# Kernel optimization log

Measured on AMD Instinct MI355X. Metric: run time of the kernel, lower is better.

## Reference

```python
import jax, jax.numpy as jnp
import numpy as np

EMB = 2048
N_HEADS = 16
HEAD_DIM = EMB // N_HEADS
ROPE_BASE = 10000.0


def _rope_cos_sin(seq_len, head_dim, dtype):
    inv_freq = 1.0 / (ROPE_BASE ** (jnp.arange(0, head_dim, 2, dtype=jnp.float32) / head_dim))
    t = jnp.arange(seq_len, dtype=jnp.float32)
    freqs = jnp.einsum('s,d->sd', t, inv_freq)          # [S, head_dim/2]
    emb = jnp.concatenate([freqs, freqs], axis=-1)       # [S, head_dim]
    return jnp.cos(emb).astype(dtype), jnp.sin(emb).astype(dtype)


def _rotate_half(x):
    x1, x2 = jnp.split(x, 2, axis=-1)
    return jnp.concatenate([-x2, x1], axis=-1)


def _apply_rope(x, cos, sin):
    # x: [B, H, S, D]; cos/sin: [S, D]
    return x * cos[None, None, :, :] + _rotate_half(x) * sin[None, None, :, :]


def setup_inputs() -> dict:
    key = jax.random.key(0)
    k1, k2, k3 = jax.random.split(key, 3)
    B, S = 4, 2048
    x = jax.random.normal(k1, (B, S, EMB), dtype=jnp.float32)
    # Additive causal mask: 0 on/below diagonal, -1e9 above.
    causal = jnp.triu(jnp.full((S, S), -1e9, dtype=jnp.float32), k=1)
    att_mask = causal[None, None, :, :]
    Wqkv = jax.random.normal(k2, (3 * EMB, EMB), dtype=jnp.float32) * (EMB ** -0.5)
    Wout = jax.random.normal(k3, (EMB, EMB), dtype=jnp.float32) * (EMB ** -0.5)
    return {"x": x, "att_mask": att_mask, "Wqkv": Wqkv, "Wout": Wout}


def reference(x, att_mask, Wqkv, Wout):
    B, S, E = x.shape
    qkv = jnp.einsum('bse,fe->bsf', x, Wqkv)             # [B, S, 3E]
    q, k, v = jnp.split(qkv, 3, axis=-1)
    def to_heads(t):
        return t.reshape(B, S, N_HEADS, HEAD_DIM).transpose(0, 2, 1, 3)  # [B,H,S,D]
    q, k, v = to_heads(q), to_heads(k), to_heads(v)
    cos, sin = _rope_cos_sin(S, HEAD_DIM, x.dtype)
    q = _apply_rope(q, cos, sin)
    k = _apply_rope(k, cos, sin)
    scaling = HEAD_DIM ** -0.5
    dots = jnp.einsum('bhqd,bhkd->bhqk', q, k) * scaling
    dots = dots + att_mask
    attn = jax.nn.softmax(dots, axis=-1)
    out = jnp.einsum('bhqk,bhkd->bhqd', attn, v)         # [B,H,S,D]
    out = out.transpose(0, 2, 1, 3).reshape(B, S, E)
    return jnp.einsum('bse,fe->bsf', out, Wout)
```

## Files before the change

### kernel.cpp

```cpp
#include <hip/hip_runtime.h>
#include <stdint.h>

typedef __attribute__((ext_vector_type(8))) short short8_t;
typedef __attribute__((ext_vector_type(4))) float f32x4;

__device__ __forceinline__ short f2bf(float f) {
  union { float f; uint32_t u; } v; v.f = f;
  uint32_t r = v.u + 0x7FFFu + ((v.u >> 16) & 1u);
  return (short)(r >> 16);
}
__device__ __forceinline__ float bf2f(short s) {
  union { uint32_t u; float f; } v; v.u = ((uint32_t)(uint16_t)s) << 16; return v.f;
}
__device__ __forceinline__ void gld16(const void* g, void* l) {
  __builtin_amdgcn_global_load_lds((const __attribute__((address_space(1))) void*)g,
                                   (__attribute__((address_space(3))) void*)l, 16, 0, 0);
}

__global__ __launch_bounds__(256) void conv3_kernel(const float* __restrict__ x,
                                                    const float* __restrict__ wqkv,
                                                    const float* __restrict__ wout,
                                                    short* __restrict__ xb,
                                                    short* __restrict__ wqb,
                                                    short* __restrict__ woutb) {
  int i = blockIdx.x * 256 + threadIdx.x;
  const int stride = gridDim.x * 256;
  for (; i < 8388608; i += stride) {
    const float4* src;
    short4* dst;
    int j;
    if (i < 4194304) { src = (const float4*)x; dst = (short4*)xb; j = i; }
    else if (i < 7340032) { src = (const float4*)wqkv; dst = (short4*)wqb; j = i - 4194304; }
    else { src = (const float4*)wout; dst = (short4*)woutb; j = i - 7340032; }
    float4 v = src[j];
    short4 o;
    o.x = f2bf(v.x); o.y = f2bf(v.y); o.z = f2bf(v.z); o.w = f2bf(v.w);
    dst[j] = o;
  }
}

__device__ __forceinline__ void storeC(float* C, size_t i, float v) { C[i] = v; }
__device__ __forceinline__ void storeC(short* C, size_t i, float v) { C[i] = f2bf(v); }

template <typename OT, bool FUSEV>
__global__ __launch_bounds__(512, 2) void gemm8p(const short* __restrict__ A,
                                                 const short* __restrict__ B,
                                                 OT* __restrict__ C,
                                                 short* __restrict__ VT,
                                                 int M, int N, int K) {
  __shared__ __align__(16) short lds[65536];
  const int tid = threadIdx.x, lane = tid & 63, w = tid >> 6;
  const int wr = w >> 2, wc = w & 3;
  const int c = lane & 15, g4 = lane >> 4;
  const int xcd = (int)blockIdx.x & 7;
  const int t = (int)blockIdx.x >> 3;
  const int bx = (t & 7) + 8 * (t >> 5);
  const int by = xcd * 4 + ((t >> 3) & 3);
  const size_t m0 = (size_t)by * 256, n0 = (size_t)bx * 256;
  const size_t Kb = (size_t)K * 2;
  const char* Ab = (const char*)A + m0 * Kb;
  const char* Bb = (const char*)B + n0 * Kb;
  const char* aq[2];
  const char* bq[2];
#pragma unroll
  for (int i = 0; i < 2; ++i) {
    const size_t ro = (size_t)((i * 8 + w) * 16 + c) * Kb + g4 * 16;
    aq[i] = Ab + ro;
    bq[i] = Bb + ro;
  }
  char* alds = (char*)lds;
  const int aoff = wr * 8192 + lane * 16;
  const int boff = 65536 + wc * 4096 + lane * 16;
  f32x4 acc[8][4] = {};
  const int NT = K >> 6, NIT = NT >> 1;

  short8_t af[2][4], bfr[2][4];

#define STAGE(q, srcoff, ldsbase)                                  \
  gld16((q)[0] + (srcoff), alds + (ldsbase) + (w << 10));          \
  gld16((q)[1] + (srcoff), alds + (ldsbase) + ((8 + w) << 10))

  STAGE(aq, 0, 0);
  STAGE(bq, 0, 65536);
  STAGE(aq, 64, 16384);
  STAGE(bq, 64, 81920);
  STAGE(aq, 128, 32768);
  STAGE(bq, 128, 98304);
  asm volatile("s_waitcnt vmcnt(0)" ::: "memory");
  asm volatile("s_barrier" ::: "memory");

#define RD_A(S, mi, OFF) \
  asm volatile("ds_read_b128 %0, %1 offset:%c2" : "=v"(af[S][mi]) : "v"(aoff), "i"(OFF))
#define RD_B(S, ni, OFF) \
  asm volatile("ds_read_b128 %0, %1 offset:%c2" : "=v"(bfr[S][ni]) : "v"(boff), "i"(OFF))

#define PREF_A(S, BSEL, KS, MQ)                           \
  RD_A(S, 0, (BSEL) + (KS)*16384 + ((MQ)*4 + 0) * 1024);  \
  RD_A(S, 1, (BSEL) + (KS)*16384 + ((MQ)*4 + 1) * 1024);  \
  RD_A(S, 2, (BSEL) + (KS)*16384 + ((MQ)*4 + 2) * 1024);  \
  RD_A(S, 3, (BSEL) + (KS)*16384 + ((MQ)*4 + 3) * 1024)

#define PREF_B(S, BSEL, KS)                  \
  RD_B(S, 0, (BSEL) + (KS)*16384 + 0);       \
  RD_B(S, 1, (BSEL) + (KS)*16384 + 1024);    \
  RD_B(S, 2, (BSEL) + (KS)*16384 + 2048);    \
  RD_B(S, 3, (BSEL) + (KS)*16384 + 3072)

#define MFMA16(AS, BS, MQ)                                                               \
  __builtin_amdgcn_s_setprio(1);                                                         \
  _Pragma("unroll") for (int mi = 0; mi < 4; ++mi) {                                     \
    _Pragma("unroll") for (int n = 0; n < 4; ++n)                                        \
      acc[(MQ)*4 + mi][n] = __builtin_amdgcn_mfma_f32_16x16x32_bf16(                     \
          af[AS][mi], bfr[BS][n], acc[(MQ)*4 + mi][n], 0, 0, 0);                         \
  }                                                                                      \
  __builtin_amdgcn_s_setprio(0)

#define PHASE_E(AS, BS, PBSEL, PKS, q, srcoff, sbase)              \
  PREF_A(AS ^ 1, PBSEL, PKS, 1);                                   \
  STAGE(q, srcoff, sbase);                                         \
  asm volatile("s_waitcnt lgkmcnt(4)" ::: "memory");               \
  __builtin_amdgcn_sched_barrier(0);                               \
  MFMA16(AS, BS, 0);                                               \
  asm volatile("s_barrier" ::: "memory")

#define PHASE_O(AS, BS, PBSEL, PKS, q, srcoff, sbase, GATE)        \
  PREF_B(BS ^ 1, PBSEL, PKS);                                      \
  PREF_A(AS ^ 1, PBSEL, PKS, 0);                                   \
  STAGE(q, srcoff, sbase);                                         \
  asm volatile("s_waitcnt lgkmcnt(8)" ::: "memory");               \
  __builtin_amdgcn_sched_barrier(0);                               \
  MFMA16(AS, BS, 1);                                               \
  GATE;                                                            \
  asm volatile("s_barrier" ::: "memory")

#define GATE8 asm volatile("s_waitcnt vmcnt(8)" ::: "memory")
#define GATE4 asm volatile("s_waitcnt vmcnt(4)" ::: "memory")
#define NOGATE (void)0

  PREF_B(0, 0, 0);
  PREF_A(0, 0, 0, 0);

  for (int it = 0; it < NIT; ++it) {
    const int T = it << 1;
    const int t1 = (T + 1) << 7;
    const int t2 = (T + 2 < NT ? T + 2 : NT - 1) << 7;
    const int t3 = (T + 3 < NT ? T + 3 : NT - 1) << 7;
    PHASE_E(0, 0, 0, 0,      aq, t1 + 64, 49152);
    PHASE_O(1, 0, 0, 1,      bq, t1 + 64, 114688, NOGATE);
    PHASE_E(0, 1, 0, 1,      aq, t2, 0);
    PHASE_O(1, 1, 32768, 0,  bq, t2, 65536, GATE8);
    PHASE_E(0, 0, 32768, 0,  aq, t2 + 64, 16384);
    PHASE_O(1, 0, 32768, 1,  bq, t2 + 64, 81920, NOGATE);
    PHASE_E(0, 1, 32768, 1,  aq, t3, 32768);
    PHASE_O(1, 1, 0, 0,      bq, t3, 98304, GATE4);
  }
#undef PHASE_E
#undef PHASE_O
#undef GATE8
#undef GATE4
#undef NOGATE
#undef MFMA16
#undef PREF_A
#undef PREF_B
#undef RD_A
#undef RD_B
#undef STAGE

#pragma unroll
  for (int m = 0; m < 8; ++m)
#pragma unroll
    for (int n = 0; n < 4; ++n) {
      const size_t col = n0 + wc * 64 + n * 16 + c;
      const size_t rb = m0 + wr * 128 + m * 16 + g4 * 4;
      bool tovt = false;
      if constexpr (FUSEV) tovt = (col >= 4096);
      if (tovt) {
        const size_t cc = col - 4096;
        const size_t b = rb >> 11, s0 = rb & 2047;
        short4 o;
        o.x = f2bf(acc[m][n][0]); o.y = f2bf(acc[m][n][1]);
        o.z = f2bf(acc[m][n][2]); o.w = f2bf(acc[m][n][3]);
        *(short4*)&VT[(b * 2048 + cc) * 2048 + s0] = o;
      } else {
#pragma unroll
        for (int r = 0; r < 4; ++r) storeC(C, (rb + r) * (size_t)N + col, acc[m][n][r]);
      }
    }
}

__global__ __launch_bounds__(256) void rope_kernel(short* __restrict__ qkv) {
  const int g = blockIdx.x * 256 + threadIdx.x;
  const int jg = g & 7;
  const int h = (g >> 3) & 15;
  const int bs = g >> 7;
  const int s = bs & 2047;
  const size_t base = (size_t)bs * 6144 + 2048 + h * 128 + jg * 8;
  short8_t lo = *(short8_t*)&qkv[base];
  short8_t hi = *(short8_t*)&qkv[base + 64];
  short8_t olo, ohi;
#pragma unroll
  for (int t = 0; t < 8; ++t) {
    const int j = jg * 8 + t;
    const float inv = exp2f((float)j * -0.20762050593046f);
    float sn, cn;
    sincosf((float)s * inv, &sn, &cn);
    const float a = bf2f(lo[t]), b = bf2f(hi[t]);
    olo[t] = f2bf(a * cn - b * sn);
    ohi[t] = f2bf(b * cn + a * sn);
  }
  *(short8_t*)&qkv[base] = olo;
  *(short8_t*)&qkv[base + 64] = ohi;
}

__global__ __launch_bounds__(256) void attn_kernel(const short* __restrict__ qkv,
                                                   const short* __restrict__ vt,
                                                   short* __restrict__ o) {
  __shared__ __align__(16) short Kl[2][32 * 128];
  __shared__ __align__(16) short Vl[2][128 * 32];
  __shared__ __align__(16) short Pl[4][16 * 40];
  const int tid = threadIdx.x, lane = tid & 63, w = tid >> 6;
  const int c = lane & 15, g4 = lane >> 4;
  const int blk = blockIdx.x;
  const int xcd = blk & 7;
  const int l = blk >> 3;
  const int bh = xcd * 8 + (l >> 5);
  const int h = bh & 15, b = bh >> 4;
  const int q0 = (31 - (l & 31)) * 64;
  const int srow = q0 + w * 16 + c;

  short8_t qf[4];
  {
    const size_t qr = ((size_t)b * 2048 + srow) * 6144 + h * 128;
    float fl[4][8];
#pragma unroll
    for (int dc = 0; dc < 4; ++dc) {
      short8_t rawv = *(const short8_t*)&qkv[qr + dc * 32 + g4 * 8];
#pragma unroll
      for (int t = 0; t < 8; ++t) fl[dc][t] = bf2f(rawv[t]);
    }
#pragma unroll
    for (int pd = 0; pd < 2; ++pd)
#pragma unroll
      for (int t = 0; t < 8; ++t) {
        const int j = pd * 32 + g4 * 8 + t;
        const float inv = exp2f((float)j * -0.20762050593046f);
        float sn, cn;
        sincosf((float)srow * inv, &sn, &cn);
        const float a = fl[pd][t], bb = fl[pd + 2][t];
        fl[pd][t] = a * cn - bb * sn;
        fl[pd + 2][t] = bb * cn + a * sn;
      }
#pragma unroll
    for (int dc = 0; dc < 4; ++dc) {
      short8_t q8;
#pragma unroll
      for (int t = 0; t < 8; ++t) q8[t] = f2bf(fl[dc][t]);
      qf[dc] = q8;
    }
  }

  f32x4 acc_o[8] = {};
  float rs[4] = {0.f, 0.f, 0.f, 0.f};
  const float scale2 = 0.12751875222364685f;
  const char* Kbase = (const char*)qkv + ((size_t)b * 2048 * 6144 + 2048 + h * 128) * 2;
  const char* Vbase = (const char*)vt + ((size_t)(b * 16 + h) * 128 * 2048) * 2;

  const char* kq[2];
  const char* vq[2];
#pragma unroll
  for (int i = 0; i < 2; ++i) {
    const int L = ((w * 2 + i) << 10) + lane * 16;
    {
      const int row = L >> 8, inner = L & 255;
      kq[i] = Kbase + (size_t)row * 12288 + (inner ^ ((row & 7) << 4));
    }
    {
      const int row = L >> 6, inner = L & 63;
      vq[i] = Vbase + (size_t)row * 4096 + (inner ^ ((row & 3) << 4));
    }
  }
  auto stage = [&](int buf, int kv0) {
#pragma unroll
    for (int i = 0; i < 2; ++i) {
      gld16(kq[i] + (size_t)kv0 * 12288, (char*)Kl + (buf << 13) + ((w * 2 + i) << 10));
      gld16(vq[i] + (size_t)kv0 * 2, (char*)Vl + (buf << 13) + ((w * 2 + i) << 10));
    }
  };

  stage(0, 0);
  __syncthreads();
  int cur = 0;
  const int kvend = q0 + 32;
  for (int kv0 = 0; kv0 <= kvend; kv0 += 32) {
    if (kv0 <= q0) stage(cur ^ 1, kv0 + 32);
    const char* Kb = (const char*)Kl + (cur << 13);
    const char* Vb = (const char*)Vl + (cur << 13);
    const bool diag = (kv0 >= q0);
    float p[2][4];
#pragma unroll
    for (int kt = 0; kt < 2; ++kt) {
      f32x4 s4 = {};
      const int krow = kt * 16 + c;
      __builtin_amdgcn_s_setprio(1);
#pragma unroll
      for (int dc = 0; dc < 4; ++dc) {
        const int inner = (dc * 64 + g4 * 16) ^ ((krow & 7) << 4);
        short8_t kf = *(const short8_t*)(Kb + krow * 256 + inner);
        s4 = __builtin_amdgcn_mfma_f32_16x16x32_bf16(qf[dc], kf, s4, 0, 0, 0);
      }
      __builtin_amdgcn_s_setprio(0);
#pragma unroll
      for (int r = 0; r < 4; ++r) {
        float v = s4[r] * scale2 - 8.0f;
        if (diag) {
          const int kc = kv0 + kt * 16 + c;
          const int qr2 = q0 + w * 16 + g4 * 4 + r;
          if (kc > qr2) v = -1e30f;
        }
        const float pe = exp2f(v);
        p[kt][r] = pe;
        rs[r] += pe;
      }
    }
#pragma unroll
    for (int kt = 0; kt < 2; ++kt)
#pragma unroll
      for (int r = 0; r < 4; r += 2) {
        uint32_t pk;
        asm("v_cvt_pk_bf16_f32 %0, %1, %2" : "=v"(pk) : "v"(p[kt][r]), "v"(p[kt][r + 1]));
        Pl[w][(g4 * 4 + r) * 40 + kt * 16 + c] = (short)(pk & 0xffffu);
        Pl[w][(g4 * 4 + r + 1) * 40 + kt * 16 + c] = (short)(pk >> 16);
      }
    {
      short8_t pf = *(const short8_t*)&Pl[w][c * 40 + g4 * 8];
      __builtin_amdgcn_s_setprio(1);
#pragma unroll
      for (int dt = 0; dt < 8; ++dt) {
        const int vrow = dt * 16 + c;
        const int inner = (g4 * 16) ^ ((vrow & 3) << 4);
        short8_t vf = *(const short8_t*)(Vb + vrow * 64 + inner);
        acc_o[dt] = __builtin_amdgcn_mfma_f32_16x16x32_bf16(pf, vf, acc_o[dt], 0, 0, 0);
      }
      __builtin_amdgcn_s_setprio(0);
    }
    __syncthreads();
    cur ^= 1;
  }
#pragma unroll
  for (int off = 1; off < 16; off <<= 1)
#pragma unroll
    for (int r = 0; r < 4; ++r) rs[r] += __shfl_xor(rs[r], off);
  const size_t ob = ((size_t)b * 2048 + q0 + w * 16 + g4 * 4) * 2048 + h * 128;
#pragma unroll
  for (int dt = 0; dt < 8; ++dt)
#pragma unroll
    for (int r = 0; r < 4; ++r)
      o[ob + (size_t)r * 2048 + dt * 16 + c] = f2bf(acc_o[dt][r] / rs[r]);
}

extern "C" void kernel_launch(void* const* d_in, const int* in_sizes, int n_in,
                              void* d_out, int out_size, void* d_ws, size_t ws_size,
                              hipStream_t stream) {
  const float* x = (const float*)d_in[0];
  const float* Wqkv = (const float*)d_in[2];
  const float* Wout = (const float*)d_in[3];
  float* out = (float*)d_out;
  char* ws = (char*)d_ws;
  short* xb    = (short*)ws;
  short* wqb   = (short*)(ws + 33554432ull);
  short* qkv   = (short*)(ws + 58720256ull);
  short* vt    = (short*)(ws + 159383552ull);
  short* woutb = (short*)(ws + 192937984ull);
  short* attno = xb;

  conv3_kernel<<<2048, 256, 0, stream>>>(x, Wqkv, Wout, xb, wqb, woutb);
  gemm8p<short, true><<<768, 512, 0, stream>>>(xb, wqb, qkv, vt, 8192, 6144, 2048);
  rope_kernel<<<4096, 256, 0, stream>>>(qkv);
  attn_kernel<<<2048, 256, 0, stream>>>(qkv, vt, attno);
  gemm8p<float, false><<<256, 512, 0, stream>>>(attno, woutb, out, nullptr, 8192, 2048, 2048);
}
```

Baseline: 503.0 us.

## Load GEMM B operand directly into registers, stage only A through LDS

The GEMM no longer stages the B (weight) tile through LDS. Each wave loads its B fragments straight from global memory into registers, double-buffered across iterations. Only A goes through a halved LDS buffer, and the fine-grained phase pipeline with partial waitcnts is replaced by a simple two-buffer loop with __syncthreads. This cuts LDS footprint and ds_read traffic for B, but B reads are now uncoalesced per-lane global loads duplicated across the two row-waves, and lgkmcnt(0) waits serialize the LDS reads with the MFMAs.

```diff
diff --git a/kernel.cpp b/kernel.cpp
--- a/kernel.cpp
+++ b/kernel.cpp
@@ -43,12 +43,12 @@
 __device__ __forceinline__ void storeC(short* C, size_t i, float v) { C[i] = f2bf(v); }
 
 template <typename OT, bool FUSEV>
-__global__ __launch_bounds__(512, 2) void gemm8p(const short* __restrict__ A,
+__global__ __launch_bounds__(512, 2) void gemmrb(const short* __restrict__ A,
                                                  const short* __restrict__ B,
                                                  OT* __restrict__ C,
                                                  short* __restrict__ VT,
                                                  int M, int N, int K) {
-  __shared__ __align__(16) short lds[65536];
+  __shared__ __align__(16) short lds[32768];
   const int tid = threadIdx.x, lane = tid & 63, w = tid >> 6;
   const int wr = w >> 2, wc = w & 3;
   const int c = lane & 15, g4 = lane >> 4;
@@ -59,112 +59,76 @@
   const size_t m0 = (size_t)by * 256, n0 = (size_t)bx * 256;
   const size_t Kb = (size_t)K * 2;
   const char* Ab = (const char*)A + m0 * Kb;
-  const char* Bb = (const char*)B + n0 * Kb;
   const char* aq[2];
-  const char* bq[2];
-#pragma unroll
-  for (int i = 0; i < 2; ++i) {
-    const size_t ro = (size_t)((i * 8 + w) * 16 + c) * Kb + g4 * 16;
-    aq[i] = Ab + ro;
-    bq[i] = Bb + ro;
-  }
+#pragma unroll
+  for (int i = 0; i < 2; ++i) aq[i] = Ab + (size_t)((i * 8 + w) * 16 + c) * Kb + g4 * 16;
+  const char* bp = (const char*)B + (n0 + wc * 64 + c) * Kb + g4 * 16;
   char* alds = (char*)lds;
   const int aoff = wr * 8192 + lane * 16;
-  const int boff = 65536 + wc * 4096 + lane * 16;
   f32x4 acc[8][4] = {};
   const int NT = K >> 6, NIT = NT >> 1;
 
-  short8_t af[2][4], bfr[2][4];
-
-#define STAGE(q, srcoff, ldsbase)                                  \
-  gld16((q)[0] + (srcoff), alds + (ldsbase) + (w << 10));          \
-  gld16((q)[1] + (srcoff), alds + (ldsbase) + ((8 + w) << 10))
-
-  STAGE(aq, 0, 0);
-  STAGE(bq, 0, 65536);
-  STAGE(aq, 64, 16384);
-  STAGE(bq, 64, 81920);
-  STAGE(aq, 128, 32768);
-  STAGE(bq, 128, 98304);
-  asm volatile("s_waitcnt vmcnt(0)" ::: "memory");
-  asm volatile("s_barrier" ::: "memory");
-
-#define RD_A(S, mi, OFF) \
-  asm volatile("ds_read_b128 %0, %1 offset:%c2" : "=v"(af[S][mi]) : "v"(aoff), "i"(OFF))
-#define RD_B(S, ni, OFF) \
-  asm volatile("ds_read_b128 %0, %1 offset:%c2" : "=v"(bfr[S][ni]) : "v"(boff), "i"(OFF))
-
-#define PREF_A(S, BSEL, KS, MQ)                           \
-  RD_A(S, 0, (BSEL) + (KS)*16384 + ((MQ)*4 + 0) * 1024);  \
-  RD_A(S, 1, (BSEL) + (KS)*16384 + ((MQ)*4 + 1) * 1024);  \
-  RD_A(S, 2, (BSEL) + (KS)*16384 + ((MQ)*4 + 2) * 1024);  \
-  RD_A(S, 3, (BSEL) + (KS)*16384 + ((MQ)*4 + 3) * 1024)
-
-#define PREF_B(S, BSEL, KS)                  \
-  RD_B(S, 0, (BSEL) + (KS)*16384 + 0);       \
-  RD_B(S, 1, (BSEL) + (KS)*16384 + 1024);    \
-  RD_B(S, 2, (BSEL) + (KS)*16384 + 2048);    \
-  RD_B(S, 3, (BSEL) + (KS)*16384 + 3072)
-
-#define MFMA16(AS, BS, MQ)                                                               \
-  __builtin_amdgcn_s_setprio(1);                                                         \
-  _Pragma("unroll") for (int mi = 0; mi < 4; ++mi) {                                     \
-    _Pragma("unroll") for (int n = 0; n < 4; ++n)                                        \
-      acc[(MQ)*4 + mi][n] = __builtin_amdgcn_mfma_f32_16x16x32_bf16(                     \
-          af[AS][mi], bfr[BS][n], acc[(MQ)*4 + mi][n], 0, 0, 0);                         \
-  }                                                                                      \
+  short8_t af[4];
+  short8_t breg[2][4][2];
+
+#define STAGEA(BUF, KS, TOFF)                                                          \
+  gld16(aq[0] + (TOFF) + (KS) * 64, alds + (BUF) * 32768 + (KS) * 16384 + (w << 10));  \
+  gld16(aq[1] + (TOFF) + (KS) * 64, alds + (BUF) * 32768 + (KS) * 16384 + ((8 + w) << 10))
+
+#define LOADB(S, TT)                                                                   \
+  _Pragma("unroll") for (int n = 0; n < 4; ++n)                                        \
+    _Pragma("unroll") for (int ks = 0; ks < 2; ++ks)                                   \
+      breg[S][n][ks] =                                                                 \
+          *(const short8_t*)(bp + (size_t)n * 16 * Kb + (TT) * 128 + ks * 64)
+
+#define RD_A(mi, OFF) \
+  asm volatile("ds_read_b128 %0, %1 offset:%c2" : "=v"(af[mi]) : "v"(aoff), "i"(OFF))
+
+#define GRP(BUF, S, MQ, KS)                                                            \
+  RD_A(0, (BUF) * 32768 + (KS) * 16384 + ((MQ) * 4 + 0) * 1024);                       \
+  RD_A(1, (BUF) * 32768 + (KS) * 16384 + ((MQ) * 4 + 1) * 1024);                       \
+  RD_A(2, (BUF) * 32768 + (KS) * 16384 + ((MQ) * 4 + 2) * 1024);                       \
+  RD_A(3, (BUF) * 32768 + (KS) * 16384 + ((MQ) * 4 + 3) * 1024);                       \
+  asm volatile("s_waitcnt lgkmcnt(0)" ::: "memory");                                   \
+  __builtin_amdgcn_sched_barrier(0);                                                   \
+  __builtin_amdgcn_s_setprio(1);                                                       \
+  _Pragma("unroll") for (int mi = 0; mi < 4; ++mi)                                     \
+    _Pragma("unroll") for (int n = 0; n < 4; ++n)                                      \
+      acc[(MQ) * 4 + mi][n] = __builtin_amdgcn_mfma_f32_16x16x32_bf16(                 \
+          af[mi], breg[S][n][KS], acc[(MQ) * 4 + mi][n], 0, 0, 0);                     \
   __builtin_amdgcn_s_setprio(0)
 
-#define PHASE_E(AS, BS, PBSEL, PKS, q, srcoff, sbase)              \
-  PREF_A(AS ^ 1, PBSEL, PKS, 1);                                   \
-  STAGE(q, srcoff, sbase);                                         \
-  asm volatile("s_waitcnt lgkmcnt(4)" ::: "memory");               \
-  __builtin_amdgcn_sched_barrier(0);                               \
-  MFMA16(AS, BS, 0);                                               \
-  asm volatile("s_barrier" ::: "memory")
-
-#define PHASE_O(AS, BS, PBSEL, PKS, q, srcoff, sbase, GATE)        \
-  PREF_B(BS ^ 1, PBSEL, PKS);                                      \
-  PREF_A(AS ^ 1, PBSEL, PKS, 0);                                   \
-  STAGE(q, srcoff, sbase);                                         \
-  asm volatile("s_waitcnt lgkmcnt(8)" ::: "memory");               \
-  __builtin_amdgcn_sched_barrier(0);                               \
-  MFMA16(AS, BS, 1);                                               \
-  GATE;                                                            \
-  asm volatile("s_barrier" ::: "memory")
-
-#define GATE8 asm volatile("s_waitcnt vmcnt(8)" ::: "memory")
-#define GATE4 asm volatile("s_waitcnt vmcnt(4)" ::: "memory")
-#define NOGATE (void)0
-
-  PREF_B(0, 0, 0);
-  PREF_A(0, 0, 0, 0);
+#define TILE(BUF, S) \
+  GRP(BUF, S, 0, 0); \
+  GRP(BUF, S, 0, 1); \
+  GRP(BUF, S, 1, 0); \
+  GRP(BUF, S, 1, 1)
+
+  STAGEA(0, 0, 0);
+  STAGEA(0, 1, 0);
+  LOADB(0, 0);
+  __syncthreads();
 
   for (int it = 0; it < NIT; ++it) {
     const int T = it << 1;
-    const int t1 = (T + 1) << 7;
-    const int t2 = (T + 2 < NT ? T + 2 : NT - 1) << 7;
-    const int t3 = (T + 3 < NT ? T + 3 : NT - 1) << 7;
-    PHASE_E(0, 0, 0, 0,      aq, t1 + 64, 49152);
-    PHASE_O(1, 0, 0, 1,      bq, t1 + 64, 114688, NOGATE);
-    PHASE_E(0, 1, 0, 1,      aq, t2, 0);
-    PHASE_O(1, 1, 32768, 0,  bq, t2, 65536, GATE8);
-    PHASE_E(0, 0, 32768, 0,  aq, t2 + 64, 16384);
-    PHASE_O(1, 0, 32768, 1,  bq, t2 + 64, 81920, NOGATE);
-    PHASE_E(0, 1, 32768, 1,  aq, t3, 32768);
-    PHASE_O(1, 1, 0, 0,      bq, t3, 98304, GATE4);
-  }
-#undef PHASE_E
-#undef PHASE_O
-#undef GATE8
-#undef GATE4
-#undef NOGATE
-#undef MFMA16
-#undef PREF_A
-#undef PREF_B
+    const int t1 = T + 1;
+    const int t2 = (T + 2 < NT) ? T + 2 : NT - 1;
+    STAGEA(1, 0, t1 * 128);
+    STAGEA(1, 1, t1 * 128);
+    LOADB(1, t1);
+    TILE(0, 0);
+    __syncthreads();
+    STAGEA(0, 0, t2 * 128);
+    STAGEA(0, 1, t2 * 128);
+    LOADB(0, t2);
+    TILE(1, 1);
+    __syncthreads();
+  }
+#undef TILE
+#undef GRP
 #undef RD_A
-#undef RD_B
-#undef STAGE
+#undef LOADB
+#undef STAGEA
 
 #pragma unroll
   for (int m = 0; m < 8; ++m)
@@ -374,8 +338,8 @@
   short* attno = xb;
 
   conv3_kernel<<<2048, 256, 0, stream>>>(x, Wqkv, Wout, xb, wqb, woutb);
-  gemm8p<short, true><<<768, 512, 0, stream>>>(xb, wqb, qkv, vt, 8192, 6144, 2048);
+  gemmrb<short, true><<<768, 512, 0, stream>>>(xb, wqb, qkv, vt, 8192, 6144, 2048);
   rope_kernel<<<4096, 256, 0, stream>>>(qkv);
   attn_kernel<<<2048, 256, 0, stream>>>(qkv, vt, attno);
-  gemm8p<float, false><<<256, 512, 0, stream>>>(attno, woutb, out, nullptr, 8192, 2048, 2048);
-}
+  gemmrb<float, false><<<256, 512, 0, stream>>>(attno, woutb, out, nullptr, 8192, 2048, 2048);
+}
```

After: 661.8 us. 31.6% more time.
